# Kernel optimization log

Hardware: AMD Instinct MI355X
Metric: run time of the kernel (lower is better)

## Reference

```python
import jax, jax.numpy as jnp
import numpy as np

COMMITMENT_COST = 0.25
B, T, D = 32, 2048, 64
K = 1024


def setup_inputs() -> dict:
    key = jax.random.key(0)
    k1, k2 = jax.random.split(key)
    inputs = jax.random.normal(k1, (B, T, D), dtype=jnp.float32)
    # codebook init: uniform(-1/K, 1/K) in the original; use same scale
    embedding = jax.random.uniform(k2, (K, D), dtype=jnp.float32,
                                   minval=-1.0 / K, maxval=1.0 / K)
    return {"inputs": inputs, "embedding": embedding}


def reference(inputs, embedding):
    Bb, Tt, Dd = inputs.shape
    flat = inputs.reshape(-1, Dd)  # [N, D]
    dist = (jnp.sum(flat * flat, axis=1, keepdims=True)
            + jnp.sum(embedding * embedding, axis=1)[None, :]
            - 2.0 * (flat @ embedding.T))
    encoding_indices = jnp.argmin(dist, axis=1)  # [N]
    quantized = embedding[encoding_indices].reshape(Bb, Tt, Dd)
    # commitment loss: mse(stop_grad(quantized), inputs)
    e_latent_loss = jnp.mean((jax.lax.stop_gradient(quantized) - inputs) ** 2)
    vq_loss = COMMITMENT_COST * e_latent_loss
    codebook_loss = jnp.zeros((), dtype=jnp.float32)
    # straight-through estimator
    quantized_st = inputs + jax.lax.stop_gradient(quantized - inputs)
    return (quantized_st, encoding_indices.reshape(Bb, Tt),
            vq_loss, e_latent_loss, codebook_loss)
```

## Files before the change

kernel.cpp:

```cpp
#include <hip/hip_runtime.h>
#include <hip/hip_bf16.h>
#include <math.h>


typedef __attribute__((ext_vector_type(8))) short bf16x8;
typedef __attribute__((ext_vector_type(4))) float f32x4;

namespace {
constexpr int NROWS  = 65536;
constexpr int DDIM   = 64;
constexpr int KCODES = 1024;
constexpr float EPSB = 4e-5f;

constexpr size_t WS_LOSS = 0;
constexpr size_t WS_CNT  = 64;
constexpr size_t WS_SE   = 256;
constexpr size_t WS_EHB  = 8192;
constexpr size_t WS_ELB  = WS_EHB + (size_t)65536 * 2;
constexpr size_t WS_BIDX = WS_ELB + (size_t)65536 * 2;
constexpr size_t WS_LIST = WS_BIDX + (size_t)NROWS * 4;
constexpr size_t WS_KEY  = WS_LIST + (size_t)NROWS * 4;
constexpr size_t WS_MV   = WS_KEY + (size_t)NROWS * 8;
constexpr size_t WS_KV   = WS_MV + (size_t)4 * NROWS * 8;
}

__device__ inline short f2bf(float v) {
  __hip_bfloat16 h = __float2bfloat16(v);
  return *reinterpret_cast<short*>(&h);
}
__device__ inline float bf2f(short s) {
  __hip_bfloat16 h;
  *reinterpret_cast<short*>(&h) = s;
  return __bfloat162float(h);
}
__device__ inline f32x4 mfma16(bf16x8 a, bf16x8 b, f32x4 c) {
  return __builtin_amdgcn_mfma_f32_16x16x32_bf16(a, b, c, 0, 0, 0);
}
__device__ inline unsigned int fflip(unsigned int b) {
  return b ^ ((unsigned int)((int)b >> 31) | 0x80000000u);
}

__global__ __launch_bounds__(256) void vq_prep(const float* __restrict__ emb,
                                               float* __restrict__ se,
                                               short* __restrict__ ehB,
                                               short* __restrict__ elB,
                                               unsigned long long* __restrict__ keyBest,
                                               double* __restrict__ loss_accum,
                                               int* __restrict__ cnt) {
  #pragma clang fp contract(off)
  const int gid = blockIdx.x * 256 + (int)threadIdx.x;
  if (gid == 0) { *loss_accum = 0.0; *cnt = 0; }
  keyBest[gid] = ~0ull;

  if (gid < KCODES) {
    const float* e = emb + (size_t)gid * DDIM;
    float r[8];
    #pragma unroll
    for (int j = 0; j < 8; ++j) r[j] = e[j] * e[j];
    #pragma unroll
    for (int i = 8; i < DDIM; i += 8) {
      #pragma unroll
      for (int j = 0; j < 8; ++j) r[j] += e[i + j] * e[i + j];
    }
    se[gid] = ((r[0] + r[1]) + (r[2] + r[3])) + ((r[4] + r[5]) + (r[6] + r[7]));
  }

  if (gid < 8192) {
    const int t  = gid >> 7;
    const int dc = (gid >> 6) & 1;
    const int l  = gid & 63;
    const int code = t * 16 + (l & 15);
    const int d0   = dc * 32 + (l >> 4) * 8;
    const float* ep = emb + (size_t)code * DDIM + d0;
    const size_t ob = ((size_t)(t * 2 + dc) * 64 + l) * 8;
    #pragma unroll
    for (int i = 0; i < 8; ++i) {
      const float v = ep[i];
      const short h = f2bf(v);
      ehB[ob + i] = h;
      elB[ob + i] = f2bf(v - bf2f(h));
    }
  }
}

__global__ __launch_bounds__(256, 2) void vq_fused(const float* __restrict__ x,
                                                   const short* __restrict__ ehB,
                                                   const short* __restrict__ elB,
                                                   const float* __restrict__ se,
                                                   float2* __restrict__ mv,
                                                   unsigned long long* __restrict__ kv) {
  #pragma clang fp contract(off)
  __shared__ float sel[256];
  const int tid  = (int)threadIdx.x;
  const int l    = tid & 63;
  const int wid  = tid >> 6;
  const int quar = (int)blockIdx.x & 3;
  const int rblk = (int)blockIdx.x >> 2;
  const int t0   = quar * 16;
  sel[tid] = se[t0 * 16 + tid];
  __syncthreads();

  const int wrb = rblk * 128 + wid * 32;
  bf16x8 xh[2][2], xl[2][2];
  #pragma unroll
  for (int rt = 0; rt < 2; ++rt) {
    const float* xp = x + (size_t)(wrb + rt * 16 + (l & 15)) * DDIM + (l >> 4) * 8;
    #pragma unroll
    for (int dc = 0; dc < 2; ++dc) {
      const float4 v0 = *reinterpret_cast<const float4*>(xp + dc * 32);
      const float4 v1 = *reinterpret_cast<const float4*>(xp + dc * 32 + 4);
      const float vv[8] = {v0.x, v0.y, v0.z, v0.w, v1.x, v1.y, v1.z, v1.w};
      #pragma unroll
      for (int i = 0; i < 8; ++i) {
        const short h = f2bf(vv[i]);
        xh[rt][dc][i] = h;
        xl[rt][dc][i] = f2bf(vv[i] - bf2f(h));
      }
    }
  }

  float m1v[2][4], m2v[2][4];
  int   m1t[2][4];
  #pragma unroll
  for (int rt = 0; rt < 2; ++rt)
    #pragma unroll
    for (int r = 0; r < 4; ++r) { m1v[rt][r] = INFINITY; m2v[rt][r] = INFINITY; m1t[rt][r] = 0; }

  const size_t lb = (size_t)l * 8;
#define FRAGLD(buf, tt, half2) \
  (*reinterpret_cast<const bf16x8*>((buf) + (size_t)(tt) * 1024 + (half2) * 512 + lb))

  bf16x8 c0 = FRAGLD(ehB, t0, 0), c1 = FRAGLD(ehB, t0, 1),
         c2 = FRAGLD(elB, t0, 0), c3 = FRAGLD(elB, t0, 1);
  bf16x8 n0 = FRAGLD(ehB, t0 + 1, 0), n1 = FRAGLD(ehB, t0 + 1, 1),
         n2 = FRAGLD(elB, t0 + 1, 0), n3 = FRAGLD(elB, t0 + 1, 1);

  const f32x4 kz = {0.f, 0.f, 0.f, 0.f};
  #pragma unroll 4
  for (int tt = 0; tt < 16; ++tt) {
    const int t = t0 + tt;
    const int tf = (tt + 2 < 16) ? t + 2 : t0 + 15;
    bf16x8 f0 = FRAGLD(ehB, tf, 0), f1 = FRAGLD(ehB, tf, 1),
           f2 = FRAGLD(elB, tf, 0), f3 = FRAGLD(elB, tf, 1);

    f32x4 a0, a1;
    a0 = mfma16(xh[0][0], c0, kz);  a1 = mfma16(xh[1][0], c0, kz);
    a0 = mfma16(xh[0][1], c1, a0);  a1 = mfma16(xh[1][1], c1, a1);
    a0 = mfma16(xh[0][0], c2, a0);  a1 = mfma16(xh[1][0], c2, a1);
    a0 = mfma16(xh[0][1], c3, a0);  a1 = mfma16(xh[1][1], c3, a1);
    a0 = mfma16(xl[0][0], c0, a0);  a1 = mfma16(xl[1][0], c0, a1);
    a0 = mfma16(xl[0][1], c1, a0);  a1 = mfma16(xl[1][1], c1, a1);

    const float sev = sel[tt * 16 + (l & 15)];
    #pragma unroll
    for (int r = 0; r < 4; ++r) {
      {
        const float d = __builtin_fmaf(-2.0f, a0[r], sev);
        const bool c = d < m1v[0][r];
        m2v[0][r] = fminf(m2v[0][r], fmaxf(m1v[0][r], d));
        m1t[0][r] = c ? t : m1t[0][r];
        m1v[0][r] = fminf(m1v[0][r], d);
      }
      {
        const float d = __builtin_fmaf(-2.0f, a1[r], sev);
        const bool c = d < m1v[1][r];
        m2v[1][r] = fminf(m2v[1][r], fmaxf(m1v[1][r], d));
        m1t[1][r] = c ? t : m1t[1][r];
        m1v[1][r] = fminf(m1v[1][r], d);
      }
    }
    c0 = n0; c1 = n1; c2 = n2; c3 = n3;
    n0 = f0; n1 = f1; n2 = f2; n3 = f3;
  }
#undef FRAGLD

  const int colbase = l & 15;
  #pragma unroll
  for (int rt = 0; rt < 2; ++rt) {
    #pragma unroll
    for (int r = 0; r < 4; ++r) {
      float m1 = m1v[rt][r], m2 = m2v[rt][r];
      unsigned long long key =
          ((unsigned long long)fflip(__float_as_uint(m1)) << 32)
          | (unsigned)(m1t[rt][r] * 16 + colbase);
      #pragma unroll
      for (int off = 1; off < 16; off <<= 1) {
        const unsigned long long ok = __shfl_xor(key, off, 16);
        const float om1 = __shfl_xor(m1, off, 16);
        const float om2 = __shfl_xor(m2, off, 16);
        m2 = fminf(fminf(m2, om2), fmaxf(m1, om1));
        m1 = fminf(m1, om1);
        key = (ok < key) ? ok : key;
      }
      if (colbase == 0) {
        const int row = wrb + rt * 16 + (l >> 4) * 4 + r;
        mv[(size_t)quar * NROWS + row] = make_float2(m1, m2);
        kv[(size_t)quar * NROWS + row] = key;
      }
    }
  }
}

__global__ __launch_bounds__(256) void vq_combine_out(const float2* __restrict__ mv,
                                                      const unsigned long long* __restrict__ kv,
                                                      const float* __restrict__ x,
                                                      const float* __restrict__ emb,
                                                      int* __restrict__ list,
                                                      int* __restrict__ cnt,
                                                      float* __restrict__ out,
                                                      double* __restrict__ loss_accum) {
  #pragma clang fp contract(off)
  __shared__ int   sbidx[256];
  __shared__ float wsum[4];
  const int tid = (int)threadIdx.x;
  const int gid = blockIdx.x * 256 + tid;
  const int l   = tid & 63;

  {
    const float2 A = mv[gid];
    const float2 B = mv[(size_t)NROWS + gid];
    const float2 C = mv[(size_t)2 * NROWS + gid];
    const float2 D = mv[(size_t)3 * NROWS + gid];
    unsigned long long kg = kv[gid];
    {
      unsigned long long k2 = kv[(size_t)NROWS + gid];     kg = (k2 < kg) ? k2 : kg;
      k2 = kv[(size_t)2 * NROWS + gid];                    kg = (k2 < kg) ? k2 : kg;
      k2 = kv[(size_t)3 * NROWS + gid];                    kg = (k2 < kg) ? k2 : kg;
    }
    const float lo1 = fminf(A.x, B.x), hi1 = fmaxf(A.x, B.x);
    const float lo2 = fminf(C.x, D.x), hi2 = fmaxf(C.x, D.x);
    const float m1g = fminf(lo1, lo2);
    const float sec = fminf(fmaxf(lo1, lo2), fminf(hi1, hi2));
    const float m2g = fminf(sec, fminf(fminf(A.y, B.y), fminf(C.y, D.y)));
    const bool cert = m2g > m1g + EPSB;
    sbidx[tid] = cert ? (int)(kg & 0xffffffffull) : -1;

    const unsigned long long mask = __ballot(!cert);
    int base = 0;
    if (l == 0 && mask) base = atomicAdd(cnt, (int)__popcll(mask));
    base = __shfl(base, 0, 64);
    if (!cert) {
      const int off = (int)__popcll(mask & ((1ull << l) - 1ull));
      list[base + off] = gid;
    }
  }
  __syncthreads();

  const int wid = tid >> 6;
  const int sub = l >> 4;
  const int q16 = l & 15;
  float lacc = 0.f;

  for (int it = 0; it < 16; ++it) {
    const int rloc = it * 16 + wid * 4 + sub;
    const int bi = sbidx[rloc];
    if (bi < 0) continue;
    const int row = blockIdx.x * 256 + rloc;
    const float4 xv = reinterpret_cast<const float4*>(x)[(size_t)row * 16 + q16];
    const float4 ev = reinterpret_cast<const float4*>(emb)[(size_t)bi * 16 + q16];
    const float da = ev.x - xv.x;
    const float db = ev.y - xv.y;
    const float dc = ev.z - xv.z;
    const float dd = ev.w - xv.w;
    float4 o;
    o.x = xv.x + da; o.y = xv.y + db; o.z = xv.z + dc; o.w = xv.w + dd;
    reinterpret_cast<float4*>(out)[(size_t)row * 16 + q16] = o;
    lacc += da * da + db * db + dc * dc + dd * dd;
    if (q16 == 0) out[(size_t)NROWS * DDIM + row] = (float)bi;
  }
  #pragma unroll
  for (int off = 32; off > 0; off >>= 1) lacc += __shfl_down(lacc, off, 64);
  if (l == 0) wsum[wid] = lacc;
  __syncthreads();
  if (tid == 0)
    atomicAdd(loss_accum, (double)(wsum[0] + wsum[1] + wsum[2] + wsum[3]));
}

__global__ __launch_bounds__(64) void vq_exact(const float* __restrict__ x,
                                               const float* __restrict__ emb,
                                               const float* __restrict__ se,
                                               const int* __restrict__ list,
                                               const int* __restrict__ cnt,
                                               unsigned long long* __restrict__ keyBest) {
  #pragma clang fp contract(off)
  __shared__ __align__(16) float eL[32 * DDIM];
  const int n = *cnt;
  if (n == 0) return;
  const int nrb = (n + 63) >> 6;
  const int ntasks = nrb * 32;
  const int l = (int)threadIdx.x;

  for (int t = (int)blockIdx.x; t < ntasks; t += (int)gridDim.x) {
    const int part = t & 31;
    const int rb   = t >> 5;
    const int j0   = part * 32;

    {
      const float4* src = reinterpret_cast<const float4*>(emb + (size_t)j0 * DDIM);
      float4* dst = reinterpret_cast<float4*>(eL);
      #pragma unroll
      for (int i = 0; i < 8; ++i) dst[i * 64 + l] = src[i * 64 + l];
    }
    __syncthreads();

    const int idx = rb * 64 + l;
    const bool act = idx < n;
    const int row = act ? list[idx] : 0;
    const float4* xr4 = reinterpret_cast<const float4*>(x + (size_t)row * DDIM);

    float xv[DDIM];
    #pragma unroll
    for (int q = 0; q < 16; ++q) {
      const float4 v = xr4[q];
      xv[q * 4 + 0] = v.x; xv[q * 4 + 1] = v.y;
      xv[q * 4 + 2] = v.z; xv[q * 4 + 3] = v.w;
    }

    float rr[8];
    #pragma unroll
    for (int j = 0; j < 8; ++j) rr[j] = xv[j] * xv[j];
    #pragma unroll
    for (int i = 8; i < DDIM; i += 8) {
      #pragma unroll
      for (int j = 0; j < 8; ++j) rr[j] += xv[i + j] * xv[i + j];
    }
    const float sx = ((rr[0] + rr[1]) + (rr[2] + rr[3])) + ((rr[4] + rr[5]) + (rr[6] + rr[7]));

    unsigned long long best = ~0ull;
    #pragma unroll 1
    for (int g = 0; g < 8; ++g) {
      const int jb = g * 4;
      const float4* e0 = reinterpret_cast<const float4*>(eL + (jb + 0) * DDIM);
      const float4* e1 = reinterpret_cast<const float4*>(eL + (jb + 1) * DDIM);
      const float4* e2 = reinterpret_cast<const float4*>(eL + (jb + 2) * DDIM);
      const float4* e3 = reinterpret_cast<const float4*>(eL + (jb + 3) * DDIM);
      float a0 = 0.f, a1 = 0.f, a2 = 0.f, a3 = 0.f;
      #pragma unroll
      for (int q = 0; q < 16; ++q) {
        const float4 v0 = e0[q], v1 = e1[q], v2 = e2[q], v3 = e3[q];
        const float xa = xv[q * 4 + 0], xb = xv[q * 4 + 1];
        const float xc = xv[q * 4 + 2], xd = xv[q * 4 + 3];
        a0 = __builtin_fmaf(xa, v0.x, a0); a0 = __builtin_fmaf(xb, v0.y, a0);
        a0 = __builtin_fmaf(xc, v0.z, a0); a0 = __builtin_fmaf(xd, v0.w, a0);
        a1 = __builtin_fmaf(xa, v1.x, a1); a1 = __builtin_fmaf(xb, v1.y, a1);
        a1 = __builtin_fmaf(xc, v1.z, a1); a1 = __builtin_fmaf(xd, v1.w, a1);
        a2 = __builtin_fmaf(xa, v2.x, a2); a2 = __builtin_fmaf(xb, v2.y, a2);
        a2 = __builtin_fmaf(xc, v2.z, a2); a2 = __builtin_fmaf(xd, v2.w, a2);
        a3 = __builtin_fmaf(xa, v3.x, a3); a3 = __builtin_fmaf(xb, v3.y, a3);
        a3 = __builtin_fmaf(xc, v3.z, a3); a3 = __builtin_fmaf(xd, v3.w, a3);
      }
      const int j = j0 + jb;
      const float T0 = sx + se[j + 0];
      const float T1 = sx + se[j + 1];
      const float T2 = sx + se[j + 2];
      const float T3 = sx + se[j + 3];
      const float di0 = __builtin_fmaf(-2.0f, a0, T0);
      const float di1 = __builtin_fmaf(-2.0f, a1, T1);
      const float di2 = __builtin_fmaf(-2.0f, a2, T2);
      const float di3 = __builtin_fmaf(-2.0f, a3, T3);
      unsigned long long k;
      k = ((unsigned long long)fflip(__float_as_uint(di0)) << 32) | (unsigned)(j + 0);
      best = (k < best) ? k : best;
      k = ((unsigned long long)fflip(__float_as_uint(di1)) << 32) | (unsigned)(j + 1);
      best = (k < best) ? k : best;
      k = ((unsigned long long)fflip(__float_as_uint(di2)) << 32) | (unsigned)(j + 2);
      best = (k < best) ? k : best;
      k = ((unsigned long long)fflip(__float_as_uint(di3)) << 32) | (unsigned)(j + 3);
      best = (k < best) ? k : best;
    }
    if (act) atomicMin(&keyBest[row], best);
    __syncthreads();
  }
}

__global__ __launch_bounds__(256) void vq_minifinal(const float* __restrict__ x,
                                                    const float* __restrict__ emb,
                                                    const int* __restrict__ list,
                                                    const int* __restrict__ cnt,
                                                    const unsigned long long* __restrict__ keyBest,
                                                    float* __restrict__ out,
                                                    double* __restrict__ loss_accum) {
  #pragma clang fp contract(off)
  const int n = *cnt;
  const int l   = (int)threadIdx.x & 63;
  const int sub = l >> 4;
  const int q16 = l & 15;
  const int w   = blockIdx.x * 4 + ((int)threadIdx.x >> 6);
  const int nW  = (int)gridDim.x * 4;
  float lacc = 0.f;

  for (int base = w * 4; base < n; base += nW * 4) {
    const int i = base + sub;
    if (i >= n) continue;
    const int row = list[i];
    const int bi = (int)(keyBest[row] & 0xffffffffull);
    const float4 xv = reinterpret_cast<const float4*>(x)[(size_t)row * 16 + q16];
    const float4 ev = reinterpret_cast<const float4*>(emb)[(size_t)bi * 16 + q16];
    const float da = ev.x - xv.x;
    const float db = ev.y - xv.y;
    const float dc = ev.z - xv.z;
    const float dd = ev.w - xv.w;
    float4 o;
    o.x = xv.x + da; o.y = xv.y + db; o.z = xv.z + dc; o.w = xv.w + dd;
    reinterpret_cast<float4*>(out)[(size_t)row * 16 + q16] = o;
    lacc += da * da + db * db + dc * dc + dd * dd;
    if (q16 == 0) out[(size_t)NROWS * DDIM + row] = (float)bi;
  }
  #pragma unroll
  for (int off = 32; off > 0; off >>= 1) lacc += __shfl_down(lacc, off, 64);
  if (l == 0 && lacc != 0.f) atomicAdd(loss_accum, (double)lacc);
}

__global__ void vq_scalars(const double* __restrict__ loss_accum,
                           float* __restrict__ out) {
  if (threadIdx.x == 0 && blockIdx.x == 0) {
    const double mm = *loss_accum / (double)((size_t)NROWS * DDIM);
    const float el = (float)mm;
    float* tail = out + (size_t)NROWS * DDIM + NROWS;
    tail[0] = 0.25f * el;
    tail[1] = el;
    tail[2] = 0.0f;
  }
}

extern "C" void kernel_launch(void* const* d_in, const int* in_sizes, int n_in,
                              void* d_out, int out_size, void* d_ws, size_t ws_size,
                              hipStream_t stream) {
  const float* x   = (const float*)d_in[0];
  const float* emb = (const float*)d_in[1];
  float* out = (float*)d_out;
  char* ws = (char*)d_ws;

  double* loss_accum = (double*)(ws + WS_LOSS);
  int*    cnt        = (int*)(ws + WS_CNT);
  float*  se         = (float*)(ws + WS_SE);
  short*  ehB        = (short*)(ws + WS_EHB);
  short*  elB        = (short*)(ws + WS_ELB);
  int*    list       = (int*)(ws + WS_LIST);
  unsigned long long* keyBest = (unsigned long long*)(ws + WS_KEY);
  float2* mv         = (float2*)(ws + WS_MV);
  unsigned long long* kv = (unsigned long long*)(ws + WS_KV);

  vq_prep<<<NROWS / 256, 256, 0, stream>>>(emb, se, ehB, elB, keyBest,
                                           loss_accum, cnt);
  vq_fused<<<(NROWS / 128) * 4, 256, 0, stream>>>(x, ehB, elB, se, mv, kv);
  vq_combine_out<<<NROWS / 256, 256, 0, stream>>>(mv, kv, x, emb, list, cnt,
                                                  out, loss_accum);
  vq_exact<<<2048, 64, 0, stream>>>(x, emb, se, list, cnt, keyBest);
  vq_minifinal<<<256, 256, 0, stream>>>(x, emb, list, cnt, keyBest, out,
                                        loss_accum);
  vq_scalars<<<1, 64, 0, stream>>>(loss_accum, out);
}
```

Baseline: 94.13 us.

## Rescore ambiguous rows with only two candidates instead of full exact scan

The combine kernel now sorts the four per-quarter candidate keys and sorts ambiguous rows into two groups. Rows where only the top two quarter winners fall within the margin, and the third is clearly worse, go to a new kernel that recomputes exact fp32 distances for just those two codes. Only the remaining rows go through the full 1024-code exact scan. This cuts exact-scan work at the cost of an extra kernel launch, more list bookkeeping and atomics, and a correctness argument that relies on the per-quarter second-best bounds.

```diff
diff --git a/kernel.cpp b/kernel.cpp
--- a/kernel.cpp
+++ b/kernel.cpp
@@ -5,6 +5,7 @@
 
 typedef __attribute__((ext_vector_type(8))) short bf16x8;
 typedef __attribute__((ext_vector_type(4))) float f32x4;
+typedef unsigned long long u64;
 
 namespace {
 constexpr int NROWS  = 65536;
@@ -12,16 +13,18 @@
 constexpr int KCODES = 1024;
 constexpr float EPSB = 4e-5f;
 
-constexpr size_t WS_LOSS = 0;
-constexpr size_t WS_CNT  = 64;
-constexpr size_t WS_SE   = 256;
-constexpr size_t WS_EHB  = 8192;
-constexpr size_t WS_ELB  = WS_EHB + (size_t)65536 * 2;
-constexpr size_t WS_BIDX = WS_ELB + (size_t)65536 * 2;
-constexpr size_t WS_LIST = WS_BIDX + (size_t)NROWS * 4;
-constexpr size_t WS_KEY  = WS_LIST + (size_t)NROWS * 4;
-constexpr size_t WS_MV   = WS_KEY + (size_t)NROWS * 8;
-constexpr size_t WS_KV   = WS_MV + (size_t)4 * NROWS * 8;
+constexpr size_t WS_LOSS  = 0;
+constexpr size_t WS_CNT   = 64;
+constexpr size_t WS_SE    = 256;
+constexpr size_t WS_EHB   = 8192;
+constexpr size_t WS_ELB   = WS_EHB  + (size_t)65536 * 2;
+constexpr size_t WS_LIST  = WS_ELB  + (size_t)65536 * 2;
+constexpr size_t WS_ROWS2 = WS_LIST + (size_t)NROWS * 4;
+constexpr size_t WS_JJ2   = WS_ROWS2 + (size_t)NROWS * 4;
+constexpr size_t WS_LALL  = WS_JJ2  + (size_t)NROWS * 4;
+constexpr size_t WS_KEY   = WS_LALL + (size_t)NROWS * 4;
+constexpr size_t WS_MV    = WS_KEY  + (size_t)NROWS * 8;
+constexpr size_t WS_KV    = WS_MV   + (size_t)4 * NROWS * 8;
 }
 
 __device__ inline short f2bf(float v) {
@@ -39,17 +42,22 @@
 __device__ inline unsigned int fflip(unsigned int b) {
   return b ^ ((unsigned int)((int)b >> 31) | 0x80000000u);
 }
+__device__ inline float kval(u64 k) {
+  unsigned u = (unsigned)(k >> 32);
+  u ^= ((int)u < 0) ? 0x80000000u : 0xFFFFFFFFu;
+  return __uint_as_float(u);
+}
 
 __global__ __launch_bounds__(256) void vq_prep(const float* __restrict__ emb,
                                                float* __restrict__ se,
                                                short* __restrict__ ehB,
                                                short* __restrict__ elB,
-                                               unsigned long long* __restrict__ keyBest,
+                                               u64* __restrict__ keyBest,
                                                double* __restrict__ loss_accum,
-                                               int* __restrict__ cnt) {
+                                               int* __restrict__ cnts) {
   #pragma clang fp contract(off)
   const int gid = blockIdx.x * 256 + (int)threadIdx.x;
-  if (gid == 0) { *loss_accum = 0.0; *cnt = 0; }
+  if (gid == 0) { *loss_accum = 0.0; cnts[0] = 0; cnts[1] = 0; cnts[2] = 0; }
   keyBest[gid] = ~0ull;
 
   if (gid < KCODES) {
@@ -88,7 +96,7 @@
                                                    const short* __restrict__ elB,
                                                    const float* __restrict__ se,
                                                    float2* __restrict__ mv,
-                                                   unsigned long long* __restrict__ kv) {
+                                                   u64* __restrict__ kv) {
   #pragma clang fp contract(off)
   __shared__ float sel[256];
   const int tid  = (int)threadIdx.x;
@@ -180,12 +188,11 @@
     #pragma unroll
     for (int r = 0; r < 4; ++r) {
       float m1 = m1v[rt][r], m2 = m2v[rt][r];
-      unsigned long long key =
-          ((unsigned long long)fflip(__float_as_uint(m1)) << 32)
-          | (unsigned)(m1t[rt][r] * 16 + colbase);
+      u64 key = ((u64)fflip(__float_as_uint(m1)) << 32)
+                | (unsigned)(m1t[rt][r] * 16 + colbase);
       #pragma unroll
       for (int off = 1; off < 16; off <<= 1) {
-        const unsigned long long ok = __shfl_xor(key, off, 16);
+        const u64 ok = __shfl_xor(key, off, 16);
         const float om1 = __shfl_xor(m1, off, 16);
         const float om2 = __shfl_xor(m2, off, 16);
         m2 = fminf(fminf(m2, om2), fmaxf(m1, om1));
@@ -202,11 +209,14 @@
 }
 
 __global__ __launch_bounds__(256) void vq_combine_out(const float2* __restrict__ mv,
-                                                      const unsigned long long* __restrict__ kv,
+                                                      const u64* __restrict__ kv,
                                                       const float* __restrict__ x,
                                                       const float* __restrict__ emb,
-                                                      int* __restrict__ list,
-                                                      int* __restrict__ cnt,
+                                                      int* __restrict__ listScan,
+                                                      int* __restrict__ rows2,
+                                                      int* __restrict__ jj2,
+                                                      int* __restrict__ listAll,
+                                                      int* __restrict__ cnts,
                                                       float* __restrict__ out,
                                                       double* __restrict__ loss_accum) {
   #pragma clang fp contract(off)
@@ -221,27 +231,57 @@
     const float2 B = mv[(size_t)NROWS + gid];
     const float2 C = mv[(size_t)2 * NROWS + gid];
     const float2 D = mv[(size_t)3 * NROWS + gid];
-    unsigned long long kg = kv[gid];
+    u64 e0 = kv[gid];
+    u64 e1 = kv[(size_t)NROWS + gid];
+    u64 e2 = kv[(size_t)2 * NROWS + gid];
+    u64 e3 = kv[(size_t)3 * NROWS + gid];
+    { u64 t; if (e1 < e0) { t = e0; e0 = e1; e1 = t; } }
+    { u64 t; if (e3 < e2) { t = e2; e2 = e3; e3 = t; } }
+    { u64 t; if (e2 < e0) { t = e0; e0 = e2; e2 = t; } }
+    { u64 t; if (e3 < e1) { t = e1; e1 = e3; e3 = t; } }
+    { u64 t; if (e2 < e1) { t = e1; e1 = e2; e2 = t; } }
+    const float v1  = kval(e0);
+    const float v2k = kval(e1);
+    const float v3k = kval(e2);
+    const float mm2 = fminf(fminf(A.y, B.y), fminf(C.y, D.y));
+
+    const float m2g = fminf(v2k, mm2);
+    const bool cert = m2g > v1 + EPSB;
+    const bool twoQ = !cert && (v2k < mm2) &&
+                      (fminf(v3k, mm2) > v1 + EPSB);
+    sbidx[tid] = cert ? (int)(e0 & 0xffffffffull) : -1;
+
     {
-      unsigned long long k2 = kv[(size_t)NROWS + gid];     kg = (k2 < kg) ? k2 : kg;
-      k2 = kv[(size_t)2 * NROWS + gid];                    kg = (k2 < kg) ? k2 : kg;
-      k2 = kv[(size_t)3 * NROWS + gid];                    kg = (k2 < kg) ? k2 : kg;
-    }
-    const float lo1 = fminf(A.x, B.x), hi1 = fmaxf(A.x, B.x);
-    const float lo2 = fminf(C.x, D.x), hi2 = fmaxf(C.x, D.x);
-    const float m1g = fminf(lo1, lo2);
-    const float sec = fminf(fmaxf(lo1, lo2), fminf(hi1, hi2));
-    const float m2g = fminf(sec, fminf(fminf(A.y, B.y), fminf(C.y, D.y)));
-    const bool cert = m2g > m1g + EPSB;
-    sbidx[tid] = cert ? (int)(kg & 0xffffffffull) : -1;
-
-    const unsigned long long mask = __ballot(!cert);
-    int base = 0;
-    if (l == 0 && mask) base = atomicAdd(cnt, (int)__popcll(mask));
-    base = __shfl(base, 0, 64);
-    if (!cert) {
-      const int off = (int)__popcll(mask & ((1ull << l) - 1ull));
-      list[base + off] = gid;
+      const u64 mask = __ballot(!cert);
+      int base = 0;
+      if (l == 0 && mask) base = atomicAdd(&cnts[2], (int)__popcll(mask));
+      base = __shfl(base, 0, 64);
+      if (!cert) {
+        const int off = (int)__popcll(mask & ((1ull << l) - 1ull));
+        listAll[base + off] = gid;
+      }
+    }
+    {
+      const u64 mask = __ballot(twoQ);
+      int base = 0;
+      if (l == 0 && mask) base = atomicAdd(&cnts[1], (int)__popcll(mask));
+      base = __shfl(base, 0, 64);
+      if (twoQ) {
+        const int off = (int)__popcll(mask & ((1ull << l) - 1ull));
+        rows2[base + off] = gid;
+        jj2[base + off] = ((int)(e0 & 0xffffull) << 16) | (int)(e1 & 0xffffull);
+      }
+    }
+    {
+      const bool scan = !cert && !twoQ;
+      const u64 mask = __ballot(scan);
+      int base = 0;
+      if (l == 0 && mask) base = atomicAdd(&cnts[0], (int)__popcll(mask));
+      base = __shfl(base, 0, 64);
+      if (scan) {
+        const int off = (int)__popcll(mask & ((1ull << l) - 1ull));
+        listScan[base + off] = gid;
+      }
     }
   }
   __syncthreads();
@@ -276,15 +316,69 @@
     atomicAdd(loss_accum, (double)(wsum[0] + wsum[1] + wsum[2] + wsum[3]));
 }
 
+__global__ __launch_bounds__(256) void vq_rescore2(const float* __restrict__ x,
+                                                   const float* __restrict__ emb,
+                                                   const float* __restrict__ se,
+                                                   const int* __restrict__ rows2,
+                                                   const int* __restrict__ jj2,
+                                                   const int* __restrict__ cnts,
+                                                   u64* __restrict__ keyBest) {
+  #pragma clang fp contract(off)
+  const int n2 = cnts[1];
+  for (int idx = blockIdx.x * 256 + (int)threadIdx.x; idx < n2;
+       idx += (int)gridDim.x * 256) {
+    const int row = rows2[idx];
+    const int jj  = jj2[idx];
+    const int j1  = jj >> 16;
+    const int j2  = jj & 0xffff;
+    const float4* xr4 = reinterpret_cast<const float4*>(x + (size_t)row * DDIM);
+    const float4* e14 = reinterpret_cast<const float4*>(emb + (size_t)j1 * DDIM);
+    const float4* e24 = reinterpret_cast<const float4*>(emb + (size_t)j2 * DDIM);
+
+    float rr[8];
+    {
+      const float4 a = xr4[0], b = xr4[1];
+      rr[0] = a.x * a.x; rr[1] = a.y * a.y; rr[2] = a.z * a.z; rr[3] = a.w * a.w;
+      rr[4] = b.x * b.x; rr[5] = b.y * b.y; rr[6] = b.z * b.z; rr[7] = b.w * b.w;
+    }
+    #pragma unroll
+    for (int i = 2; i < 16; i += 2) {
+      const float4 a = xr4[i], b = xr4[i + 1];
+      rr[0] += a.x * a.x; rr[1] += a.y * a.y; rr[2] += a.z * a.z; rr[3] += a.w * a.w;
+      rr[4] += b.x * b.x; rr[5] += b.y * b.y; rr[6] += b.z * b.z; rr[7] += b.w * b.w;
+    }
+    const float sx = ((rr[0] + rr[1]) + (rr[2] + rr[3])) + ((rr[4] + rr[5]) + (rr[6] + rr[7]));
+
+    float a1 = 0.f, a2 = 0.f;
+    #pragma unroll
+    for (int q = 0; q < 16; ++q) {
+      const float4 xv = xr4[q];
+      const float4 v1 = e14[q];
+      const float4 v2 = e24[q];
+      a1 = __builtin_fmaf(xv.x, v1.x, a1); a1 = __builtin_fmaf(xv.y, v1.y, a1);
+      a1 = __builtin_fmaf(xv.z, v1.z, a1); a1 = __builtin_fmaf(xv.w, v1.w, a1);
+      a2 = __builtin_fmaf(xv.x, v2.x, a2); a2 = __builtin_fmaf(xv.y, v2.y, a2);
+      a2 = __builtin_fmaf(xv.z, v2.z, a2); a2 = __builtin_fmaf(xv.w, v2.w, a2);
+    }
+    const float T1 = sx + se[j1];
+    const float T2 = sx + se[j2];
+    const float D1 = __builtin_fmaf(-2.0f, a1, T1);
+    const float D2 = __builtin_fmaf(-2.0f, a2, T2);
+    const u64 k1 = ((u64)fflip(__float_as_uint(D1)) << 32) | (unsigned)j1;
+    const u64 k2 = ((u64)fflip(__float_as_uint(D2)) << 32) | (unsigned)j2;
+    keyBest[row] = (k1 < k2) ? k1 : k2;
+  }
+}
+
 __global__ __launch_bounds__(64) void vq_exact(const float* __restrict__ x,
                                                const float* __restrict__ emb,
                                                const float* __restrict__ se,
                                                const int* __restrict__ list,
-                                               const int* __restrict__ cnt,
-                                               unsigned long long* __restrict__ keyBest) {
+                                               const int* __restrict__ cnts,
+                                               u64* __restrict__ keyBest) {
   #pragma clang fp contract(off)
   __shared__ __align__(16) float eL[32 * DDIM];
-  const int n = *cnt;
+  const int n = cnts[0];
   if (n == 0) return;
   const int nrb = (n + 63) >> 6;
   const int ntasks = nrb * 32;
@@ -326,7 +420,7 @@
     }
     const float sx = ((rr[0] + rr[1]) + (rr[2] + rr[3])) + ((rr[4] + rr[5]) + (rr[6] + rr[7]));
 
-    unsigned long long best = ~0ull;
+    u64 best = ~0ull;
     #pragma unroll 1
     for (int g = 0; g < 8; ++g) {
       const int jb = g * 4;
@@ -358,14 +452,14 @@
       const float di1 = __builtin_fmaf(-2.0f, a1, T1);
       const float di2 = __builtin_fmaf(-2.0f, a2, T2);
       const float di3 = __builtin_fmaf(-2.0f, a3, T3);
-      unsigned long long k;
-      k = ((unsigned long long)fflip(__float_as_uint(di0)) << 32) | (unsigned)(j + 0);
+      u64 k;
+      k = ((u64)fflip(__float_as_uint(di0)) << 32) | (unsigned)(j + 0);
       best = (k < best) ? k : best;
-      k = ((unsigned long long)fflip(__float_as_uint(di1)) << 32) | (unsigned)(j + 1);
+      k = ((u64)fflip(__float_as_uint(di1)) << 32) | (unsigned)(j + 1);
       best = (k < best) ? k : best;
-      k = ((unsigned long long)fflip(__float_as_uint(di2)) << 32) | (unsigned)(j + 2);
+      k = ((u64)fflip(__float_as_uint(di2)) << 32) | (unsigned)(j + 2);
       best = (k < best) ? k : best;
-      k = ((unsigned long long)fflip(__float_as_uint(di3)) << 32) | (unsigned)(j + 3);
+      k = ((u64)fflip(__float_as_uint(di3)) << 32) | (unsigned)(j + 3);
       best = (k < best) ? k : best;
     }
     if (act) atomicMin(&keyBest[row], best);
@@ -375,13 +469,13 @@
 
 __global__ __launch_bounds__(256) void vq_minifinal(const float* __restrict__ x,
                                                     const float* __restrict__ emb,
-                                                    const int* __restrict__ list,
-                                                    const int* __restrict__ cnt,
-                                                    const unsigned long long* __restrict__ keyBest,
+                                                    const int* __restrict__ listAll,
+                                                    const int* __restrict__ cnts,
+                                                    const u64* __restrict__ keyBest,
                                                     float* __restrict__ out,
                                                     double* __restrict__ loss_accum) {
   #pragma clang fp contract(off)
-  const int n = *cnt;
+  const int n = cnts[2];
   const int l   = (int)threadIdx.x & 63;
   const int sub = l >> 4;
   const int q16 = l & 15;
@@ -392,7 +486,7 @@
   for (int base = w * 4; base < n; base += nW * 4) {
     const int i = base + sub;
     if (i >= n) continue;
-    const int row = list[i];
+    const int row = listAll[i];
     const int bi = (int)(keyBest[row] & 0xffffffffull);
     const float4 xv = reinterpret_cast<const float4*>(x)[(size_t)row * 16 + q16];
     const float4 ev = reinterpret_cast<const float4*>(emb)[(size_t)bi * 16 + q16];
@@ -432,22 +526,27 @@
   char* ws = (char*)d_ws;
 
   double* loss_accum = (double*)(ws + WS_LOSS);
-  int*    cnt        = (int*)(ws + WS_CNT);
+  int*    cnts       = (int*)(ws + WS_CNT);
   float*  se         = (float*)(ws + WS_SE);
   short*  ehB        = (short*)(ws + WS_EHB);
   short*  elB        = (short*)(ws + WS_ELB);
-  int*    list       = (int*)(ws + WS_LIST);
-  unsigned long long* keyBest = (unsigned long long*)(ws + WS_KEY);
+  int*    listScan   = (int*)(ws + WS_LIST);
+  int*    rows2      = (int*)(ws + WS_ROWS2);
+  int*    jj2        = (int*)(ws + WS_JJ2);
+  int*    listAll    = (int*)(ws + WS_LALL);
+  u64*    keyBest    = (u64*)(ws + WS_KEY);
   float2* mv         = (float2*)(ws + WS_MV);
-  unsigned long long* kv = (unsigned long long*)(ws + WS_KV);
+  u64*    kv         = (u64*)(ws + WS_KV);
 
   vq_prep<<<NROWS / 256, 256, 0, stream>>>(emb, se, ehB, elB, keyBest,
-                                           loss_accum, cnt);
+                                           loss_accum, cnts);
   vq_fused<<<(NROWS / 128) * 4, 256, 0, stream>>>(x, ehB, elB, se, mv, kv);
-  vq_combine_out<<<NROWS / 256, 256, 0, stream>>>(mv, kv, x, emb, list, cnt,
+  vq_combine_out<<<NROWS / 256, 256, 0, stream>>>(mv, kv, x, emb, listScan,
+                                                  rows2, jj2, listAll, cnts,
                                                   out, loss_accum);
-  vq_exact<<<2048, 64, 0, stream>>>(x, emb, se, list, cnt, keyBest);
-  vq_minifinal<<<256, 256, 0, stream>>>(x, emb, list, cnt, keyBest, out,
+  vq_rescore2<<<256, 256, 0, stream>>>(x, emb, se, rows2, jj2, cnts, keyBest);
+  vq_exact<<<2048, 64, 0, stream>>>(x, emb, se, listScan, cnts, keyBest);
+  vq_minifinal<<<256, 256, 0, stream>>>(x, emb, listAll, cnts, keyBest, out,
                                         loss_accum);
   vq_scalars<<<1, 64, 0, stream>>>(loss_accum, out);
 }
```

Result: slower. 110.8 us (+17.7%).
